# Optimization experiments

Measured on AMD Instinct MI355X. Metric: run time of the kernel, lower is better.

Reference implementation:

```python
import jax, jax.numpy as jnp
import numpy as np
import math

E = 1024
H = 16
D = E // H  # head_dim = 64
B, T = 2, 2048


def setup_inputs() -> dict:
    key = jax.random.key(0)
    ks = jax.random.split(key, 10)
    s_in = 1.0 / math.sqrt(E)
    s_hd = 1.0 / math.sqrt(D)
    return {
        "hidden_states": jax.random.normal(ks[0], (B, T, E), dtype=jnp.float32),
        # stacked per-head Linear weights (torch Linear: y = x @ W.T + b)
        "Wq": jax.random.uniform(ks[1], (H, E, D), jnp.float32, -s_in, s_in),
        "bq": jax.random.uniform(ks[2], (H, D), jnp.float32, -s_in, s_in),
        "Wk": jax.random.uniform(ks[3], (H, E, D), jnp.float32, -s_in, s_in),
        "bk": jax.random.uniform(ks[4], (H, D), jnp.float32, -s_in, s_in),
        "Wv": jax.random.uniform(ks[5], (H, E, D), jnp.float32, -s_in, s_in),
        "bv": jax.random.uniform(ks[6], (H, D), jnp.float32, -s_in, s_in),
        "Wo": jax.random.uniform(ks[7], (H, D, E), jnp.float32, -s_hd, s_hd),
        "bo": jax.random.uniform(ks[8], (H, E), jnp.float32, -s_hd, s_hd),
        "gate": jnp.ones((H,), dtype=jnp.float32),
    }


def reference(hidden_states, Wq, bq, Wk, bk, Wv, bv, Wo, bo, gate):
    # Batched per-head projections: [B,T,E] x [H,E,D] -> [B,H,T,D]
    Q = jnp.einsum("bte,hed->bhtd", hidden_states, Wq) + bq[None, :, None, :]
    K = jnp.einsum("bte,hed->bhtd", hidden_states, Wk) + bk[None, :, None, :]
    V = jnp.einsum("bte,hed->bhtd", hidden_states, Wv) + bv[None, :, None, :]
    scale = 1.0 / math.sqrt(D)
    scores = jnp.einsum("bhtd,bhsd->bhts", Q, K) * scale  # [B,H,T,T]
    weights = jax.nn.softmax(scores, axis=-1)
    attn = jnp.einsum("bhts,bhsd->bhtd", weights, V)  # [B,H,T,D]
    # Per-head output proj (bias included before gating), gated, summed over heads
    proj = jnp.einsum("bhtd,hde->bhte", attn, Wo) + bo[None, :, None, :]
    out = jnp.sum(proj * gate[None, :, None, None], axis=1)  # [B,T,E]
    return out
```

## Files before the change

kernel.cpp:

```cpp
#include <hip/hip_runtime.h>
#include <math.h>

#define E_DIM 1024
#define H_DIM 16
#define D_DIM 64
#define B_DIM 2
#define T_DIM 2048
#define M_TOT (B_DIM * T_DIM)

typedef __bf16 bf16_t;
typedef bf16_t bf16x4 __attribute__((ext_vector_type(4)));
typedef bf16_t bf16x8 __attribute__((ext_vector_type(8)));
typedef float f32x4 __attribute__((ext_vector_type(4)));

__device__ __forceinline__ void load_lds16(const void* g, void* l) {
    __builtin_amdgcn_global_load_lds(
        (const __attribute__((address_space(1))) unsigned int*)g,
        (__attribute__((address_space(3))) unsigned int*)l, 16, 0, 0);
}

__global__ __launch_bounds__(256) void cast_x_kernel(const float* __restrict__ x,
                                                     bf16_t* __restrict__ xb) {
    size_t i = ((size_t)blockIdx.x * 256 + threadIdx.x) * 8;
    float4 a = *reinterpret_cast<const float4*>(x + i);
    float4 b = *reinterpret_cast<const float4*>(x + i + 4);
    bf16x8 o;
    o[0] = (bf16_t)a.x; o[1] = (bf16_t)a.y; o[2] = (bf16_t)a.z; o[3] = (bf16_t)a.w;
    o[4] = (bf16_t)b.x; o[5] = (bf16_t)b.y; o[6] = (bf16_t)b.z; o[7] = (bf16_t)b.w;
    *reinterpret_cast<bf16x8*>(xb + i) = o;
}

__global__ __launch_bounds__(256) void wqkv_t_kernel(
    const float* __restrict__ Wq, const float* __restrict__ Wk,
    const float* __restrict__ Wv, bf16_t* __restrict__ Wcat) {
    const int et = blockIdx.x, h = blockIdx.y, z = blockIdx.z;
    const float* W = z == 0 ? Wq : (z == 1 ? Wk : Wv);
    __shared__ float Tt[64][65];
    const int tid = threadIdx.x;
    const int r = tid >> 2, c4 = (tid & 3) * 16;
    const float* src = W + (size_t)h * 65536 + (size_t)(et * 64 + r) * 64 + c4;
    #pragma unroll
    for (int k = 0; k < 16; k += 4) {
        float4 v = *reinterpret_cast<const float4*>(src + k);
        Tt[r][c4 + k + 0] = v.x; Tt[r][c4 + k + 1] = v.y;
        Tt[r][c4 + k + 2] = v.z; Tt[r][c4 + k + 3] = v.w;
    }
    __syncthreads();
    bf16x8 o0, o1;
    #pragma unroll
    for (int k = 0; k < 8; ++k) o0[k] = (bf16_t)Tt[c4 + k][r];
    #pragma unroll
    for (int k = 0; k < 8; ++k) o1[k] = (bf16_t)Tt[c4 + 8 + k][r];
    bf16_t* dst = Wcat + ((size_t)(z * 16 + h) * 64 + r) * 1024 + et * 64 + c4;
    *reinterpret_cast<bf16x8*>(dst) = o0;
    *reinterpret_cast<bf16x8*>(dst + 8) = o1;
}

__global__ __launch_bounds__(256) void wo_t_kernel(const float* __restrict__ Wo,
                                                   const float* __restrict__ gate,
                                                   bf16_t* __restrict__ Wgt) {
    const int et = blockIdx.x, h = blockIdx.y;
    const float g = gate[h];
    __shared__ float Tt[64][65];
    const int tid = threadIdx.x;
    const int r = tid >> 2, c4 = (tid & 3) * 16;
    const float* src = Wo + (size_t)h * 65536 + (size_t)r * 1024 + et * 64 + c4;
    #pragma unroll
    for (int k = 0; k < 16; k += 4) {
        float4 v = *reinterpret_cast<const float4*>(src + k);
        Tt[r][c4 + k + 0] = v.x * g; Tt[r][c4 + k + 1] = v.y * g;
        Tt[r][c4 + k + 2] = v.z * g; Tt[r][c4 + k + 3] = v.w * g;
    }
    __syncthreads();
    bf16x8 o0, o1;
    #pragma unroll
    for (int k = 0; k < 8; ++k) o0[k] = (bf16_t)Tt[c4 + k][r];
    #pragma unroll
    for (int k = 0; k < 8; ++k) o1[k] = (bf16_t)Tt[c4 + 8 + k][r];
    bf16_t* dst = Wgt + (size_t)(et * 64 + r) * 1024 + h * 64 + c4;
    *reinterpret_cast<bf16x8*>(dst) = o0;
    *reinterpret_cast<bf16x8*>(dst + 8) = o1;
}

__global__ __launch_bounds__(256) void bias_sum_kernel(const float* __restrict__ bo,
                                                       const float* __restrict__ gate,
                                                       float* __restrict__ bsum) {
    int e = blockIdx.x * 256 + threadIdx.x;
    float s = 0.f;
    #pragma unroll
    for (int h = 0; h < H_DIM; ++h) s += gate[h] * bo[h * E_DIM + e];
    bsum[e] = s;
}

__global__ __launch_bounds__(256) void qkv_gemm_kernel(
    const bf16_t* __restrict__ Xb, const bf16_t* __restrict__ Wcat,
    const float* __restrict__ bqp, const float* __restrict__ bkp,
    const float* __restrict__ bvp,
    bf16_t* __restrict__ Qw, bf16_t* __restrict__ Kw, bf16_t* __restrict__ Vtw) {
    const int p = blockIdx.x;
    const int l = (p & 7) * 96 + (p >> 3);
    const int mx = l & 31, ny = l >> 5;
    const int m0 = mx * 128, n0 = ny * 128;

    __shared__ bf16_t As[128][32];
    __shared__ bf16_t Bs[128][32];

    const int tid = threadIdx.x;
    const int lane = tid & 63, wid = tid >> 6;
    const int wr = wid >> 1, wc = wid & 1;
    const int lr = lane & 15, lg = lane >> 4;
    const int srow = lane >> 2, scol = (lane & 3) * 8;

    f32x4 acc[4][4] = {};

    for (int k0 = 0; k0 < E_DIM; k0 += 32) {
        #pragma unroll
        for (int j = 0; j < 2; ++j) {
            load_lds16(Xb + (size_t)(m0 + wid * 32 + j * 16 + srow) * E_DIM + k0 + scol,
                       (char*)&As[0][0] + wid * 2048 + j * 1024);
            load_lds16(Wcat + (size_t)(n0 + wid * 32 + j * 16 + srow) * E_DIM + k0 + scol,
                       (char*)&Bs[0][0] + wid * 2048 + j * 1024);
        }
        __syncthreads();
        bf16x8 a[4], b[4];
        #pragma unroll
        for (int i = 0; i < 4; ++i)
            a[i] = *reinterpret_cast<const bf16x8*>(&As[wr * 64 + i * 16 + lr][lg * 8]);
        #pragma unroll
        for (int j = 0; j < 4; ++j)
            b[j] = *reinterpret_cast<const bf16x8*>(&Bs[wc * 64 + j * 16 + lr][lg * 8]);
        __builtin_amdgcn_s_setprio(1);
        #pragma unroll
        for (int i = 0; i < 4; ++i)
            #pragma unroll
            for (int j = 0; j < 4; ++j)
                acc[i][j] = __builtin_amdgcn_mfma_f32_16x16x32_bf16(a[i], b[j], acc[i][j], 0, 0, 0);
        __builtin_amdgcn_s_setprio(0);
        __syncthreads();
    }

    const int z = n0 >> 10;
    const float scale = (z == 0) ? 0.125f : 1.0f;
    const float* bias = z == 0 ? bqp : (z == 1 ? bkp : bvp);
    const int b_idx = m0 >> 11;
    const int t00 = m0 & (T_DIM - 1);

    #pragma unroll
    for (int j = 0; j < 4; ++j) {
        const int n = n0 + wc * 64 + j * 16 + lr;
        const int h = (n >> 6) & 15;
        const int d = n & 63;
        const float bval = bias[n & 1023];
        if (z != 2) {
            bf16_t* O = (z == 0 ? Qw : Kw) + (size_t)(b_idx * H_DIM + h) * T_DIM * 64;
            #pragma unroll
            for (int i = 0; i < 4; ++i)
                #pragma unroll
                for (int r = 0; r < 4; ++r) {
                    int t = t00 + wr * 64 + i * 16 + lg * 4 + r;
                    O[(size_t)t * 64 + d] = (bf16_t)((acc[i][j][r] + bval) * scale);
                }
        } else {
            bf16_t* O = Vtw + (size_t)(b_idx * H_DIM + h) * 64 * T_DIM + (size_t)d * T_DIM;
            #pragma unroll
            for (int i = 0; i < 4; ++i) {
                int t = t00 + wr * 64 + i * 16 + lg * 4;
                bf16x4 t4;
                #pragma unroll
                for (int r = 0; r < 4; ++r) t4[r] = (bf16_t)(acc[i][j][r] + bval);
                *reinterpret_cast<bf16x4*>(&O[t]) = t4;
            }
        }
    }
}

__global__ __launch_bounds__(512, 4) void attn_mfma_kernel(
    const bf16_t* __restrict__ Q, const bf16_t* __restrict__ K,
    const bf16_t* __restrict__ Vt, bf16_t* __restrict__ Aw) {
    const int p = blockIdx.x;
    const int l = (p & 7) * 64 + (p >> 3);
    const int qx = l & 15, bh = l >> 4;
    const int b_idx = bh >> 4, h = bh & 15;
    const int q0 = qx * 128;
    const size_t base = (size_t)bh * T_DIM * 64;

    __shared__ bf16_t Ks[128][72];
    __shared__ bf16_t Vs[64][136];
    __shared__ bf16_t Ps[8][16][136];

    const int tid = threadIdx.x;
    const int lane = tid & 63;
    const int wid = tid >> 6;
    const int lr = lane & 15, lg = lane >> 4;

    bf16x8 bq[2];
    #pragma unroll
    for (int kc = 0; kc < 2; ++kc)
        bq[kc] = *reinterpret_cast<const bf16x8*>(
            Q + base + (size_t)(q0 + wid * 16 + lr) * 64 + kc * 32 + lg * 8);

    float mreg = -INFINITY, lrow = 0.f;
    f32x4 o[4] = {};

    for (int s0 = 0; s0 < T_DIM; s0 += 128) {
        {
            const int kr = tid >> 2, kc = (tid & 3) * 16;
            const bf16_t* ksrc = K + base + (size_t)(s0 + kr) * 64 + kc;
            *reinterpret_cast<bf16x8*>(&Ks[kr][kc])     = *reinterpret_cast<const bf16x8*>(ksrc);
            *reinterpret_cast<bf16x8*>(&Ks[kr][kc + 8]) = *reinterpret_cast<const bf16x8*>(ksrc + 8);
            const int vr = tid >> 3, vc = (tid & 7) * 16;
            const bf16_t* vsrc = Vt + base + (size_t)vr * T_DIM + s0 + vc;
            *reinterpret_cast<bf16x8*>(&Vs[vr][vc])     = *reinterpret_cast<const bf16x8*>(vsrc);
            *reinterpret_cast<bf16x8*>(&Vs[vr][vc + 8]) = *reinterpret_cast<const bf16x8*>(vsrc + 8);
        }
        __syncthreads();

        f32x4 s[8] = {};
        __builtin_amdgcn_s_setprio(1);
        #pragma unroll
        for (int kb = 0; kb < 8; ++kb)
            #pragma unroll
            for (int kc = 0; kc < 2; ++kc) {
                bf16x8 ak = *reinterpret_cast<const bf16x8*>(&Ks[kb * 16 + lr][kc * 32 + lg * 8]);
                s[kb] = __builtin_amdgcn_mfma_f32_16x16x32_bf16(ak, bq[kc], s[kb], 0, 0, 0);
            }
        __builtin_amdgcn_s_setprio(0);

        float pmax = -INFINITY;
        #pragma unroll
        for (int kb = 0; kb < 8; ++kb) {
            float m01 = fmaxf(s[kb][0], s[kb][1]);
            float m23 = fmaxf(s[kb][2], s[kb][3]);
            pmax = fmaxf(pmax, fmaxf(m01, m23));
        }
        pmax = fmaxf(pmax, __shfl_xor(pmax, 16));
        pmax = fmaxf(pmax, __shfl_xor(pmax, 32));

        if (__any(pmax > mreg + 8.f)) {
            float newm = fmaxf(mreg, pmax);
            float alpha = __expf(mreg - newm);
            mreg = newm;
            lrow *= alpha;
            #pragma unroll
            for (int r = 0; r < 4; ++r) {
                float ar = __shfl(alpha, lg * 4 + r);
                o[0][r] *= ar; o[1][r] *= ar; o[2][r] *= ar; o[3][r] *= ar;
            }
        }

        float rs = 0.f;
        #pragma unroll
        for (int kb = 0; kb < 8; ++kb) {
            bf16x4 t4;
            #pragma unroll
            for (int r = 0; r < 4; ++r) {
                float pv = __expf(s[kb][r] - mreg);
                rs += pv;
                t4[r] = (bf16_t)pv;
            }
            *reinterpret_cast<bf16x4*>(&Ps[wid][lr][kb * 16 + lg * 4]) = t4;
        }
        rs += __shfl_xor(rs, 16);
        rs += __shfl_xor(rs, 32);
        lrow += rs;

        asm volatile("s_waitcnt lgkmcnt(0)" ::: "memory");

        __builtin_amdgcn_s_setprio(1);
        #pragma unroll
        for (int sc = 0; sc < 4; ++sc) {
            bf16x8 ap = *reinterpret_cast<const bf16x8*>(&Ps[wid][lr][sc * 32 + lg * 8]);
            #pragma unroll
            for (int nd = 0; nd < 4; ++nd) {
                bf16x8 bv = *reinterpret_cast<const bf16x8*>(&Vs[nd * 16 + lr][sc * 32 + lg * 8]);
                o[nd] = __builtin_amdgcn_mfma_f32_16x16x32_bf16(ap, bv, o[nd], 0, 0, 0);
            }
        }
        __builtin_amdgcn_s_setprio(0);
        __syncthreads();
    }

    #pragma unroll
    for (int r = 0; r < 4; ++r) {
        float lsum = __shfl(lrow, lg * 4 + r);
        float linv = 1.f / lsum;
        int t = q0 + wid * 16 + lg * 4 + r;
        size_t rowbase = ((size_t)b_idx * T_DIM + t) * E_DIM + h * 64;
        #pragma unroll
        for (int nd = 0; nd < 4; ++nd)
            Aw[rowbase + nd * 16 + lr] = (bf16_t)(o[nd][r] * linv);
    }
}

__global__ __launch_bounds__(256) void out_gemm_kernel(
    const bf16_t* __restrict__ Aw, const bf16_t* __restrict__ Wgt,
    const float* __restrict__ bsum, float* __restrict__ out) {
    const int p = blockIdx.x;
    const int l = (p & 7) * 32 + (p >> 3);
    const int mx = l & 31, ny = l >> 5;
    const int m0 = mx * 128, n0 = ny * 128;

    __shared__ bf16_t As[128][32];
    __shared__ bf16_t Bs[128][32];

    const int tid = threadIdx.x;
    const int lane = tid & 63, wid = tid >> 6;
    const int wr = wid >> 1, wc = wid & 1;
    const int lr = lane & 15, lg = lane >> 4;
    const int srow = lane >> 2, scol = (lane & 3) * 8;

    f32x4 acc[4][4] = {};

    for (int k0 = 0; k0 < E_DIM; k0 += 32) {
        #pragma unroll
        for (int j = 0; j < 2; ++j) {
            load_lds16(Aw + (size_t)(m0 + wid * 32 + j * 16 + srow) * E_DIM + k0 + scol,
                       (char*)&As[0][0] + wid * 2048 + j * 1024);
            load_lds16(Wgt + (size_t)(n0 + wid * 32 + j * 16 + srow) * E_DIM + k0 + scol,
                       (char*)&Bs[0][0] + wid * 2048 + j * 1024);
        }
        __syncthreads();
        bf16x8 a[4], b[4];
        #pragma unroll
        for (int i = 0; i < 4; ++i)
            a[i] = *reinterpret_cast<const bf16x8*>(&As[wr * 64 + i * 16 + lr][lg * 8]);
        #pragma unroll
        for (int j = 0; j < 4; ++j)
            b[j] = *reinterpret_cast<const bf16x8*>(&Bs[wc * 64 + j * 16 + lr][lg * 8]);
        __builtin_amdgcn_s_setprio(1);
        #pragma unroll
        for (int i = 0; i < 4; ++i)
            #pragma unroll
            for (int j = 0; j < 4; ++j)
                acc[i][j] = __builtin_amdgcn_mfma_f32_16x16x32_bf16(a[i], b[j], acc[i][j], 0, 0, 0);
        __builtin_amdgcn_s_setprio(0);
        __syncthreads();
    }

    #pragma unroll
    for (int j = 0; j < 4; ++j) {
        const int e = n0 + wc * 64 + j * 16 + lr;
        const float be = bsum[e];
        #pragma unroll
        for (int i = 0; i < 4; ++i)
            #pragma unroll
            for (int r = 0; r < 4; ++r) {
                int m = m0 + wr * 64 + i * 16 + lg * 4 + r;
                out[(size_t)m * E_DIM + e] = acc[i][j][r] + be;
            }
    }
}

extern "C" void kernel_launch(void* const* d_in, const int* in_sizes, int n_in,
                              void* d_out, int out_size, void* d_ws, size_t ws_size,
                              hipStream_t stream) {
    const float* hs   = (const float*)d_in[0];
    const float* Wq   = (const float*)d_in[1];
    const float* bq   = (const float*)d_in[2];
    const float* Wk   = (const float*)d_in[3];
    const float* bk   = (const float*)d_in[4];
    const float* Wv   = (const float*)d_in[5];
    const float* bv   = (const float*)d_in[6];
    const float* Wo   = (const float*)d_in[7];
    const float* bo   = (const float*)d_in[8];
    const float* gate = (const float*)d_in[9];
    float* out = (float*)d_out;

    const size_t NX = (size_t)M_TOT * E_DIM;
    const size_t NW = (size_t)H_DIM * D_DIM * E_DIM;
    bf16_t* p = (bf16_t*)d_ws;
    bf16_t* Xb   = p; p += NX;
    bf16_t* Wcat = p; p += 3 * NW;
    bf16_t* Wgt  = p; p += NW;
    bf16_t* Qw   = p; p += NX;
    bf16_t* Kw   = p; p += NX;
    bf16_t* Vtw  = p; p += NX;
    bf16_t* Aw   = p; p += NX;
    float*  bsum = (float*)p;

    cast_x_kernel<<<dim3(NX / 2048), 256, 0, stream>>>(hs, Xb);
    wqkv_t_kernel<<<dim3(16, 16, 3), 256, 0, stream>>>(Wq, Wk, Wv, Wcat);
    wo_t_kernel<<<dim3(16, 16), 256, 0, stream>>>(Wo, gate, Wgt);
    bias_sum_kernel<<<dim3(4), 256, 0, stream>>>(bo, gate, bsum);

    qkv_gemm_kernel<<<dim3(768), 256, 0, stream>>>(Xb, Wcat, bq, bk, bv, Qw, Kw, Vtw);

    attn_mfma_kernel<<<dim3(512), 512, 0, stream>>>(Qw, Kw, Vtw, Aw);

    out_gemm_kernel<<<dim3(256), 256, 0, stream>>>(Aw, Wgt, bsum, out);
}
```

Measured before the change: 215.9 us.

## Double-buffer GEMM and attention K/V loads, vectorize epilogues, use exp2 softmax

The QKV GEMM is split into a Q/K kernel and a V kernel. All GEMMs now double-buffer their LDS tiles with a single barrier per k-step, and the Q/K and output GEMMs swap MFMA operand order so that the epilogues can write vectorized rows. The attention kernel prefetches the next K/V tile into registers while computing on the current one, folds log2(e) into the Q scale so it can use exp2f, raises the lazy-rescale threshold to match, and writes its output with vector stores. The cost is more LDS and registers, and the bigger rescale threshold could affect accuracy.

```diff
diff --git a/kernel.cpp b/kernel.cpp
--- a/kernel.cpp
+++ b/kernel.cpp
@@ -12,6 +12,8 @@
 typedef bf16_t bf16x4 __attribute__((ext_vector_type(4)));
 typedef bf16_t bf16x8 __attribute__((ext_vector_type(8)));
 typedef float f32x4 __attribute__((ext_vector_type(4)));
+
+#define LOG2E_DIV8 0.18033688011112042f
 
 __device__ __forceinline__ void load_lds16(const void* g, void* l) {
     __builtin_amdgcn_global_load_lds(
@@ -92,18 +94,17 @@
     bsum[e] = s;
 }
 
-__global__ __launch_bounds__(256) void qkv_gemm_kernel(
+__global__ __launch_bounds__(256) void qk_gemm_kernel(
     const bf16_t* __restrict__ Xb, const bf16_t* __restrict__ Wcat,
     const float* __restrict__ bqp, const float* __restrict__ bkp,
-    const float* __restrict__ bvp,
-    bf16_t* __restrict__ Qw, bf16_t* __restrict__ Kw, bf16_t* __restrict__ Vtw) {
+    bf16_t* __restrict__ Qw, bf16_t* __restrict__ Kw) {
     const int p = blockIdx.x;
-    const int l = (p & 7) * 96 + (p >> 3);
+    const int l = (p & 7) * 64 + (p >> 3);
     const int mx = l & 31, ny = l >> 5;
     const int m0 = mx * 128, n0 = ny * 128;
 
-    __shared__ bf16_t As[128][32];
-    __shared__ bf16_t Bs[128][32];
+    __shared__ bf16_t As[2][128][32];
+    __shared__ bf16_t Bs[2][128][32];
 
     const int tid = threadIdx.x;
     const int lane = tid & 63, wid = tid >> 6;
@@ -113,63 +114,130 @@
 
     f32x4 acc[4][4] = {};
 
-    for (int k0 = 0; k0 < E_DIM; k0 += 32) {
-        #pragma unroll
-        for (int j = 0; j < 2; ++j) {
-            load_lds16(Xb + (size_t)(m0 + wid * 32 + j * 16 + srow) * E_DIM + k0 + scol,
-                       (char*)&As[0][0] + wid * 2048 + j * 1024);
-            load_lds16(Wcat + (size_t)(n0 + wid * 32 + j * 16 + srow) * E_DIM + k0 + scol,
-                       (char*)&Bs[0][0] + wid * 2048 + j * 1024);
-        }
+    #define STAGE_QK(buf, k0)                                                      \
+        _Pragma("unroll")                                                          \
+        for (int j = 0; j < 2; ++j) {                                              \
+            load_lds16(Xb + (size_t)(m0 + wid * 32 + j * 16 + srow) * E_DIM + (k0) + scol, \
+                       (char*)&As[buf][0][0] + wid * 2048 + j * 1024);             \
+            load_lds16(Wcat + (size_t)(n0 + wid * 32 + j * 16 + srow) * E_DIM + (k0) + scol, \
+                       (char*)&Bs[buf][0][0] + wid * 2048 + j * 1024);             \
+        }
+
+    STAGE_QK(0, 0);
+    for (int t = 0; t < 32; ++t) {
         __syncthreads();
-        bf16x8 a[4], b[4];
+        if (t < 31) STAGE_QK((t + 1) & 1, (t + 1) * 32);
+        const int b = t & 1;
+        bf16x8 a[4], bb[4];
         #pragma unroll
         for (int i = 0; i < 4; ++i)
-            a[i] = *reinterpret_cast<const bf16x8*>(&As[wr * 64 + i * 16 + lr][lg * 8]);
+            a[i] = *reinterpret_cast<const bf16x8*>(&As[b][wr * 64 + i * 16 + lr][lg * 8]);
         #pragma unroll
         for (int j = 0; j < 4; ++j)
-            b[j] = *reinterpret_cast<const bf16x8*>(&Bs[wc * 64 + j * 16 + lr][lg * 8]);
+            bb[j] = *reinterpret_cast<const bf16x8*>(&Bs[b][wc * 64 + j * 16 + lr][lg * 8]);
         __builtin_amdgcn_s_setprio(1);
         #pragma unroll
-        for (int i = 0; i < 4; ++i)
-            #pragma unroll
-            for (int j = 0; j < 4; ++j)
-                acc[i][j] = __builtin_amdgcn_mfma_f32_16x16x32_bf16(a[i], b[j], acc[i][j], 0, 0, 0);
+        for (int j = 0; j < 4; ++j)
+            #pragma unroll
+            for (int i = 0; i < 4; ++i)
+                acc[j][i] = __builtin_amdgcn_mfma_f32_16x16x32_bf16(bb[j], a[i], acc[j][i], 0, 0, 0);
         __builtin_amdgcn_s_setprio(0);
-        __syncthreads();
-    }
+    }
+    #undef STAGE_QK
 
     const int z = n0 >> 10;
-    const float scale = (z == 0) ? 0.125f : 1.0f;
-    const float* bias = z == 0 ? bqp : (z == 1 ? bkp : bvp);
+    const float scale = (z == 0) ? LOG2E_DIV8 : 1.0f;
+    const float* bias = (z == 0) ? bqp : bkp;
+    bf16_t* Obase = (z == 0) ? Qw : Kw;
     const int b_idx = m0 >> 11;
     const int t00 = m0 & (T_DIM - 1);
 
+    #pragma unroll
+    for (int j = 0; j < 4; ++j) {
+        const int n = n0 + wc * 64 + j * 16 + lg * 4;
+        const int h = (n >> 6) & 15;
+        const int dbase = (n & 63);
+        const float4 bv4 = *reinterpret_cast<const float4*>(&bias[n & 1023]);
+        bf16_t* O = Obase + (size_t)(b_idx * H_DIM + h) * T_DIM * 64;
+        #pragma unroll
+        for (int i = 0; i < 4; ++i) {
+            const int t = t00 + wr * 64 + i * 16 + lr;
+            bf16x4 t4;
+            #pragma unroll
+            for (int r = 0; r < 4; ++r)
+                t4[r] = (bf16_t)((acc[j][i][r] + (&bv4.x)[r]) * scale);
+            *reinterpret_cast<bf16x4*>(&O[(size_t)t * 64 + dbase]) = t4;
+        }
+    }
+}
+
+__global__ __launch_bounds__(256) void v_gemm_kernel(
+    const bf16_t* __restrict__ Xb, const bf16_t* __restrict__ Wcat,
+    const float* __restrict__ bvp, bf16_t* __restrict__ Vtw) {
+    const int p = blockIdx.x;
+    const int l = (p & 7) * 32 + (p >> 3);
+    const int mx = l & 31, ny = l >> 5;
+    const int m0 = mx * 128, n0 = ny * 128;
+    const bf16_t* Wv = Wcat + (size_t)2048 * E_DIM;
+
+    __shared__ bf16_t As[2][128][32];
+    __shared__ bf16_t Bs[2][128][32];
+
+    const int tid = threadIdx.x;
+    const int lane = tid & 63, wid = tid >> 6;
+    const int wr = wid >> 1, wc = wid & 1;
+    const int lr = lane & 15, lg = lane >> 4;
+    const int srow = lane >> 2, scol = (lane & 3) * 8;
+
+    f32x4 acc[4][4] = {};
+
+    #define STAGE_V(buf, k0)                                                       \
+        _Pragma("unroll")                                                          \
+        for (int j = 0; j < 2; ++j) {                                              \
+            load_lds16(Xb + (size_t)(m0 + wid * 32 + j * 16 + srow) * E_DIM + (k0) + scol, \
+                       (char*)&As[buf][0][0] + wid * 2048 + j * 1024);             \
+            load_lds16(Wv + (size_t)(n0 + wid * 32 + j * 16 + srow) * E_DIM + (k0) + scol, \
+                       (char*)&Bs[buf][0][0] + wid * 2048 + j * 1024);             \
+        }
+
+    STAGE_V(0, 0);
+    for (int t = 0; t < 32; ++t) {
+        __syncthreads();
+        if (t < 31) STAGE_V((t + 1) & 1, (t + 1) * 32);
+        const int b = t & 1;
+        bf16x8 a[4], bb[4];
+        #pragma unroll
+        for (int i = 0; i < 4; ++i)
+            a[i] = *reinterpret_cast<const bf16x8*>(&As[b][wr * 64 + i * 16 + lr][lg * 8]);
+        #pragma unroll
+        for (int j = 0; j < 4; ++j)
+            bb[j] = *reinterpret_cast<const bf16x8*>(&Bs[b][wc * 64 + j * 16 + lr][lg * 8]);
+        __builtin_amdgcn_s_setprio(1);
+        #pragma unroll
+        for (int i = 0; i < 4; ++i)
+            #pragma unroll
+            for (int j = 0; j < 4; ++j)
+                acc[i][j] = __builtin_amdgcn_mfma_f32_16x16x32_bf16(a[i], bb[j], acc[i][j], 0, 0, 0);
+        __builtin_amdgcn_s_setprio(0);
+    }
+    #undef STAGE_V
+
+    const int b_idx = m0 >> 11;
+    const int t00 = m0 & (T_DIM - 1);
     #pragma unroll
     for (int j = 0; j < 4; ++j) {
         const int n = n0 + wc * 64 + j * 16 + lr;
         const int h = (n >> 6) & 15;
         const int d = n & 63;
-        const float bval = bias[n & 1023];
-        if (z != 2) {
-            bf16_t* O = (z == 0 ? Qw : Kw) + (size_t)(b_idx * H_DIM + h) * T_DIM * 64;
-            #pragma unroll
-            for (int i = 0; i < 4; ++i)
-                #pragma unroll
-                for (int r = 0; r < 4; ++r) {
-                    int t = t00 + wr * 64 + i * 16 + lg * 4 + r;
-                    O[(size_t)t * 64 + d] = (bf16_t)((acc[i][j][r] + bval) * scale);
-                }
-        } else {
-            bf16_t* O = Vtw + (size_t)(b_idx * H_DIM + h) * 64 * T_DIM + (size_t)d * T_DIM;
-            #pragma unroll
-            for (int i = 0; i < 4; ++i) {
-                int t = t00 + wr * 64 + i * 16 + lg * 4;
-                bf16x4 t4;
-                #pragma unroll
-                for (int r = 0; r < 4; ++r) t4[r] = (bf16_t)(acc[i][j][r] + bval);
-                *reinterpret_cast<bf16x4*>(&O[t]) = t4;
-            }
+        const float bval = bvp[n];
+        bf16_t* O = Vtw + (size_t)(b_idx * H_DIM + h) * 64 * T_DIM + (size_t)d * T_DIM;
+        #pragma unroll
+        for (int i = 0; i < 4; ++i) {
+            const int t = t00 + wr * 64 + i * 16 + lg * 4;
+            bf16x4 t4;
+            #pragma unroll
+            for (int r = 0; r < 4; ++r) t4[r] = (bf16_t)(acc[i][j][r] + bval);
+            *reinterpret_cast<bf16x4*>(&O[t]) = t4;
         }
     }
 }
@@ -199,21 +267,37 @@
         bq[kc] = *reinterpret_cast<const bf16x8*>(
             Q + base + (size_t)(q0 + wid * 16 + lr) * 64 + kc * 32 + lg * 8);
 
+    const int kr = tid >> 2, kc0 = (tid & 3) * 16;
+    const int vr = tid >> 3, vc0 = (tid & 7) * 16;
+
+    bf16x8 kA, kB, vA, vB;
+    {
+        const bf16_t* ksrc = K + base + (size_t)kr * 64 + kc0;
+        kA = *reinterpret_cast<const bf16x8*>(ksrc);
+        kB = *reinterpret_cast<const bf16x8*>(ksrc + 8);
+        const bf16_t* vsrc = Vt + base + (size_t)vr * T_DIM + vc0;
+        vA = *reinterpret_cast<const bf16x8*>(vsrc);
+        vB = *reinterpret_cast<const bf16x8*>(vsrc + 8);
+        *reinterpret_cast<bf16x8*>(&Ks[kr][kc0])     = kA;
+        *reinterpret_cast<bf16x8*>(&Ks[kr][kc0 + 8]) = kB;
+        *reinterpret_cast<bf16x8*>(&Vs[vr][vc0])     = vA;
+        *reinterpret_cast<bf16x8*>(&Vs[vr][vc0 + 8]) = vB;
+    }
+    __syncthreads();
+
     float mreg = -INFINITY, lrow = 0.f;
     f32x4 o[4] = {};
 
     for (int s0 = 0; s0 < T_DIM; s0 += 128) {
-        {
-            const int kr = tid >> 2, kc = (tid & 3) * 16;
-            const bf16_t* ksrc = K + base + (size_t)(s0 + kr) * 64 + kc;
-            *reinterpret_cast<bf16x8*>(&Ks[kr][kc])     = *reinterpret_cast<const bf16x8*>(ksrc);
-            *reinterpret_cast<bf16x8*>(&Ks[kr][kc + 8]) = *reinterpret_cast<const bf16x8*>(ksrc + 8);
-            const int vr = tid >> 3, vc = (tid & 7) * 16;
-            const bf16_t* vsrc = Vt + base + (size_t)vr * T_DIM + s0 + vc;
-            *reinterpret_cast<bf16x8*>(&Vs[vr][vc])     = *reinterpret_cast<const bf16x8*>(vsrc);
-            *reinterpret_cast<bf16x8*>(&Vs[vr][vc + 8]) = *reinterpret_cast<const bf16x8*>(vsrc + 8);
-        }
-        __syncthreads();
+        const bool more = (s0 + 128) < T_DIM;
+        if (more) {
+            const bf16_t* ksrc = K + base + (size_t)(s0 + 128 + kr) * 64 + kc0;
+            kA = *reinterpret_cast<const bf16x8*>(ksrc);
+            kB = *reinterpret_cast<const bf16x8*>(ksrc + 8);
+            const bf16_t* vsrc = Vt + base + (size_t)vr * T_DIM + s0 + 128 + vc0;
+            vA = *reinterpret_cast<const bf16x8*>(vsrc);
+            vB = *reinterpret_cast<const bf16x8*>(vsrc + 8);
+        }
 
         f32x4 s[8] = {};
         __builtin_amdgcn_s_setprio(1);
@@ -236,16 +320,13 @@
         pmax = fmaxf(pmax, __shfl_xor(pmax, 16));
         pmax = fmaxf(pmax, __shfl_xor(pmax, 32));
 
-        if (__any(pmax > mreg + 8.f)) {
+        if (__any(pmax > mreg + 11.5f)) {
             float newm = fmaxf(mreg, pmax);
-            float alpha = __expf(mreg - newm);
+            float alpha = exp2f(mreg - newm);
             mreg = newm;
             lrow *= alpha;
             #pragma unroll
-            for (int r = 0; r < 4; ++r) {
-                float ar = __shfl(alpha, lg * 4 + r);
-                o[0][r] *= ar; o[1][r] *= ar; o[2][r] *= ar; o[3][r] *= ar;
-            }
+            for (int db = 0; db < 4; ++db) o[db] *= alpha;
         }
 
         float rs = 0.f;
@@ -254,7 +335,7 @@
             bf16x4 t4;
             #pragma unroll
             for (int r = 0; r < 4; ++r) {
-                float pv = __expf(s[kb][r] - mreg);
+                float pv = exp2f(s[kb][r] - mreg);
                 rs += pv;
                 t4[r] = (bf16_t)pv;
             }
@@ -264,31 +345,37 @@
         rs += __shfl_xor(rs, 32);
         lrow += rs;
 
-        asm volatile("s_waitcnt lgkmcnt(0)" ::: "memory");
-
         __builtin_amdgcn_s_setprio(1);
         #pragma unroll
         for (int sc = 0; sc < 4; ++sc) {
-            bf16x8 ap = *reinterpret_cast<const bf16x8*>(&Ps[wid][lr][sc * 32 + lg * 8]);
-            #pragma unroll
-            for (int nd = 0; nd < 4; ++nd) {
-                bf16x8 bv = *reinterpret_cast<const bf16x8*>(&Vs[nd * 16 + lr][sc * 32 + lg * 8]);
-                o[nd] = __builtin_amdgcn_mfma_f32_16x16x32_bf16(ap, bv, o[nd], 0, 0, 0);
+            bf16x8 bp = *reinterpret_cast<const bf16x8*>(&Ps[wid][lr][sc * 32 + lg * 8]);
+            #pragma unroll
+            for (int db = 0; db < 4; ++db) {
+                bf16x8 av = *reinterpret_cast<const bf16x8*>(&Vs[db * 16 + lr][sc * 32 + lg * 8]);
+                o[db] = __builtin_amdgcn_mfma_f32_16x16x32_bf16(av, bp, o[db], 0, 0, 0);
             }
         }
         __builtin_amdgcn_s_setprio(0);
         __syncthreads();
-    }
-
-    #pragma unroll
-    for (int r = 0; r < 4; ++r) {
-        float lsum = __shfl(lrow, lg * 4 + r);
-        float linv = 1.f / lsum;
-        int t = q0 + wid * 16 + lg * 4 + r;
-        size_t rowbase = ((size_t)b_idx * T_DIM + t) * E_DIM + h * 64;
-        #pragma unroll
-        for (int nd = 0; nd < 4; ++nd)
-            Aw[rowbase + nd * 16 + lr] = (bf16_t)(o[nd][r] * linv);
+
+        if (more) {
+            *reinterpret_cast<bf16x8*>(&Ks[kr][kc0])     = kA;
+            *reinterpret_cast<bf16x8*>(&Ks[kr][kc0 + 8]) = kB;
+            *reinterpret_cast<bf16x8*>(&Vs[vr][vc0])     = vA;
+            *reinterpret_cast<bf16x8*>(&Vs[vr][vc0 + 8]) = vB;
+        }
+        __syncthreads();
+    }
+
+    const float linv = 1.f / lrow;
+    const int t = q0 + wid * 16 + lr;
+    const size_t rowbase = ((size_t)b_idx * T_DIM + t) * E_DIM + h * 64;
+    #pragma unroll
+    for (int db = 0; db < 4; ++db) {
+        bf16x4 t4;
+        #pragma unroll
+        for (int r = 0; r < 4; ++r) t4[r] = (bf16_t)(o[db][r] * linv);
+        *reinterpret_cast<bf16x4*>(&Aw[rowbase + db * 16 + lg * 4]) = t4;
     }
 }
 
@@ -300,8 +387,8 @@
     const int mx = l & 31, ny = l >> 5;
     const int m0 = mx * 128, n0 = ny * 128;
 
-    __shared__ bf16_t As[128][32];
-    __shared__ bf16_t Bs[128][32];
+    __shared__ bf16_t As[2][128][32];
+    __shared__ bf16_t Bs[2][128][32];
 
     const int tid = threadIdx.x;
     const int lane = tid & 63, wid = tid >> 6;
@@ -311,43 +398,51 @@
 
     f32x4 acc[4][4] = {};
 
-    for (int k0 = 0; k0 < E_DIM; k0 += 32) {
-        #pragma unroll
-        for (int j = 0; j < 2; ++j) {
-            load_lds16(Aw + (size_t)(m0 + wid * 32 + j * 16 + srow) * E_DIM + k0 + scol,
-                       (char*)&As[0][0] + wid * 2048 + j * 1024);
-            load_lds16(Wgt + (size_t)(n0 + wid * 32 + j * 16 + srow) * E_DIM + k0 + scol,
-                       (char*)&Bs[0][0] + wid * 2048 + j * 1024);
-        }
+    #define STAGE_O(buf, k0)                                                       \
+        _Pragma("unroll")                                                          \
+        for (int j = 0; j < 2; ++j) {                                              \
+            load_lds16(Aw + (size_t)(m0 + wid * 32 + j * 16 + srow) * E_DIM + (k0) + scol, \
+                       (char*)&As[buf][0][0] + wid * 2048 + j * 1024);             \
+            load_lds16(Wgt + (size_t)(n0 + wid * 32 + j * 16 + srow) * E_DIM + (k0) + scol, \
+                       (char*)&Bs[buf][0][0] + wid * 2048 + j * 1024);             \
+        }
+
+    STAGE_O(0, 0);
+    for (int t = 0; t < 32; ++t) {
         __syncthreads();
-        bf16x8 a[4], b[4];
+        if (t < 31) STAGE_O((t + 1) & 1, (t + 1) * 32);
+        const int b = t & 1;
+        bf16x8 a[4], bb[4];
         #pragma unroll
         for (int i = 0; i < 4; ++i)
-            a[i] = *reinterpret_cast<const bf16x8*>(&As[wr * 64 + i * 16 + lr][lg * 8]);
+            a[i] = *reinterpret_cast<const bf16x8*>(&As[b][wr * 64 + i * 16 + lr][lg * 8]);
         #pragma unroll
         for (int j = 0; j < 4; ++j)
-            b[j] = *reinterpret_cast<const bf16x8*>(&Bs[wc * 64 + j * 16 + lr][lg * 8]);
+            bb[j] = *reinterpret_cast<const bf16x8*>(&Bs[b][wc * 64 + j * 16 + lr][lg * 8]);
         __builtin_amdgcn_s_setprio(1);
         #pragma unroll
-        for (int i = 0; i < 4; ++i)
-            #pragma unroll
-            for (int j = 0; j < 4; ++j)
-                acc[i][j] = __builtin_amdgcn_mfma_f32_16x16x32_bf16(a[i], b[j], acc[i][j], 0, 0, 0);
+        for (int j = 0; j < 4; ++j)
+            #pragma unroll
+            for (int i = 0; i < 4; ++i)
+                acc[j][i] = __builtin_amdgcn_mfma_f32_16x16x32_bf16(bb[j], a[i], acc[j][i], 0, 0, 0);
         __builtin_amdgcn_s_setprio(0);
-        __syncthreads();
-    }
+    }
+    #undef STAGE_O
 
     #pragma unroll
     for (int j = 0; j < 4; ++j) {
-        const int e = n0 + wc * 64 + j * 16 + lr;
-        const float be = bsum[e];
-        #pragma unroll
-        for (int i = 0; i < 4; ++i)
-            #pragma unroll
-            for (int r = 0; r < 4; ++r) {
-                int m = m0 + wr * 64 + i * 16 + lg * 4 + r;
-                out[(size_t)m * E_DIM + e] = acc[i][j][r] + be;
-            }
+        const int e = n0 + wc * 64 + j * 16 + lg * 4;
+        const float4 bs4 = *reinterpret_cast<const float4*>(&bsum[e]);
+        #pragma unroll
+        for (int i = 0; i < 4; ++i) {
+            const int m = m0 + wr * 64 + i * 16 + lr;
+            float4 o4;
+            o4.x = acc[j][i][0] + bs4.x;
+            o4.y = acc[j][i][1] + bs4.y;
+            o4.z = acc[j][i][2] + bs4.z;
+            o4.w = acc[j][i][3] + bs4.w;
+            *reinterpret_cast<float4*>(&out[(size_t)m * E_DIM + e]) = o4;
+        }
     }
 }
 
@@ -383,7 +478,8 @@
     wo_t_kernel<<<dim3(16, 16), 256, 0, stream>>>(Wo, gate, Wgt);
     bias_sum_kernel<<<dim3(4), 256, 0, stream>>>(bo, gate, bsum);
 
-    qkv_gemm_kernel<<<dim3(768), 256, 0, stream>>>(Xb, Wcat, bq, bk, bv, Qw, Kw, Vtw);
+    qk_gemm_kernel<<<dim3(512), 256, 0, stream>>>(Xb, Wcat, bq, bk, Qw, Kw);
+    v_gemm_kernel<<<dim3(256), 256, 0, stream>>>(Xb, Wcat, bv, Vtw);
 
     attn_mfma_kernel<<<dim3(512), 512, 0, stream>>>(Qw, Kw, Vtw, Aw);
 
```

After: 250.7 us. 16.1% more time.
